# Kernel tuning notes

Hardware: AMD Instinct MI355X
Metric: run time of the kernel (lower is better)

Reference implementation:

```python
import jax, jax.numpy as jnp
import numpy as np

EMBED_DIM = 1024
NUM_HEADS = 16
HEAD_DIM = EMBED_DIM // NUM_HEADS


def setup_inputs() -> dict:
    key = jax.random.key(0)
    ks = jax.random.split(key, 10)
    B, S, E = 2, 2048, EMBED_DIM
    scale = 1.0 / np.sqrt(E)
    x = jax.random.normal(ks[0], (B, S, E), dtype=jnp.float32)
    mask = jax.random.randint(ks[1], (B, 1, S, S), 0, 2, dtype=jnp.int32)
    # Linear weights stored as [in, out] (transposed torch layout for x @ W)
    Wq = jax.random.normal(ks[2], (E, E), dtype=jnp.float32) * scale
    bq = jnp.zeros((E,), dtype=jnp.float32)
    Wk = jax.random.normal(ks[3], (E, E), dtype=jnp.float32) * scale
    bk = jnp.zeros((E,), dtype=jnp.float32)
    Wv = jax.random.normal(ks[4], (E, E), dtype=jnp.float32) * scale
    bv = jnp.zeros((E,), dtype=jnp.float32)
    Wo = jax.random.normal(ks[5], (E, E), dtype=jnp.float32) * scale
    bo = jnp.zeros((E,), dtype=jnp.float32)
    return {"x": x, "mask": mask, "Wq": Wq, "bq": bq, "Wk": Wk, "bk": bk,
            "Wv": Wv, "bv": bv, "Wo": Wo, "bo": bo}


def _heads(t, B, S):
    # [B, S, E] -> [B, H, S, Dh]
    return t.reshape(B, S, NUM_HEADS, HEAD_DIM).transpose(0, 2, 1, 3)


def reference(x, mask, Wq, bq, Wk, bk, Wv, bv, Wo, bo):
    B, S, E = x.shape
    q = _heads(x @ Wq + bq, B, S)
    k = _heads(x @ Wk + bk, B, S)
    v = _heads(x @ Wv + bv, B, S)
    inv_sqrt_dk = 1.0 / jnp.sqrt(jnp.asarray(HEAD_DIM, dtype=x.dtype))
    # scores: [B, H, S, S]
    scores = jnp.einsum('bhqd,bhkd->bhqk', q, k) * inv_sqrt_dk
    scores = jnp.where(mask == 0, jnp.asarray(-1e9, dtype=scores.dtype), scores)
    p = jax.nn.softmax(scores, axis=-1)
    ctx = jnp.einsum('bhqk,bhkd->bhqd', p, v)  # [B, H, S, Dh]
    ctx = ctx.transpose(0, 2, 1, 3).reshape(B, S, E)
    return ctx @ Wo + bo
```

## Files before the change

### kernel.cpp

```cpp
#include <hip/hip_runtime.h>

typedef float f32x4 __attribute__((ext_vector_type(4)));
typedef short s16x8 __attribute__((ext_vector_type(8)));
typedef unsigned short u16;
typedef unsigned short u16x4 __attribute__((ext_vector_type(4)));
typedef unsigned int u32x2 __attribute__((ext_vector_type(2)));

#define DI __device__ __forceinline__

constexpr int B_ = 2, S_ = 2048, E_ = 1024, H_ = 16, DH = 64, M_ = B_ * S_;
constexpr float QSCALE = 0.125f * 1.4426950408889634f;

DI u16 f2bf(float f) {
    unsigned u = __float_as_uint(f);
    u += 0x7fffu + ((u >> 16) & 1u);
    return (u16)(u >> 16);
}

DI unsigned cvtpk(float lo, float hi) {
    unsigned r;
    asm("v_cvt_pk_bf16_f32 %0, %1, %2" : "=v"(r) : "v"(lo), "v"(hi));
    return r;
}

DI float max3f(float a, float b, float c) {
    float r;
    asm("v_max3_f32 %0, %1, %2, %3" : "=v"(r) : "v"(a), "v"(b), "v"(c));
    return r;
}

DI void mfma(f32x4& d, s16x8 a, s16x8 b) {
    asm("v_mfma_f32_16x16x32_bf16 %0, %1, %2, %0" : "+v"(d) : "v"(a), "v"(b));
}

typedef __attribute__((address_space(1))) const void gas_cv;
typedef __attribute__((address_space(3))) void las_v;
DI void gl16(const void* g, void* l) {
    __builtin_amdgcn_global_load_lds((gas_cv*)g, (las_v*)l, 16, 0, 0);
}

__global__ __launch_bounds__(256) void prep(const float* __restrict__ x,
                                            u16* __restrict__ xb,
                                            const float* __restrict__ Wq,
                                            const float* __restrict__ Wk,
                                            const float* __restrict__ Wv,
                                            const float* __restrict__ Wo,
                                            u16* __restrict__ Wqkvt,
                                            u16* __restrict__ Wot,
                                            const int* __restrict__ mask,
                                            u32x2* __restrict__ mc) {
    __shared__ float t[64][65];
    const int bid = blockIdx.x;
    if (bid < 4096) {
        int i = bid * 256 + threadIdx.x;
        float4 v = ((const float4*)x)[i];
        u16x4 o;
        o.x = f2bf(v.x); o.y = f2bf(v.y); o.z = f2bf(v.z); o.w = f2bf(v.w);
        ((u16x4*)xb)[i] = o;
    } else if (bid < 5120) {
        const int wb = bid - 4096, w = wb >> 8, rem = wb & 255;
        const float* in = (w == 0) ? Wq : (w == 1) ? Wk : (w == 2) ? Wv : Wo;
        u16* out = (w == 3) ? Wot : Wqkvt + w * 1024 * 1024;
        const int k0 = (rem & 15) * 64, n0 = (rem >> 4) * 64;
        const int tx = threadIdx.x & 63, ty = threadIdx.x >> 6;
#pragma unroll
        for (int i = 0; i < 16; i++) {
            int r = i * 4 + ty;
            t[r][tx] = in[(k0 + r) * E_ + n0 + tx];
        }
        __syncthreads();
#pragma unroll
        for (int i = 0; i < 16; i++) {
            int r = i * 4 + ty;
            out[(n0 + r) * E_ + k0 + tx] = f2bf(t[tx][r]);
        }
    } else {
        const int bq = bid - 5120;
        const int b = bq >> 7, qt = bq & 127;
        const int tid = threadIdx.x, lane = tid & 63, w = tid >> 6;
        const int lr = lane & 15, g = lane >> 4;
        const int* mrow = mask + ((size_t)(b * S_ + qt * 16 + lr)) * S_;
        u32x2* ob = mc + (size_t)bq * 32 * 4 * 64 + lane;
        for (int kt = w; kt < 32; kt += 4) {
#pragma unroll
            for (int n = 0; n < 4; n++) {
                int4 mv = *(const int4*)(mrow + kt * 64 + n * 16 + g * 4);
                u32x2 e;
                e.x = (mv.x ? 0xFFFFu : 0u) | (mv.y ? 0xFFFF0000u : 0u);
                e.y = (mv.z ? 0xFFFFu : 0u) | (mv.w ? 0xFFFF0000u : 0u);
                ob[(kt * 4 + n) * 64] = e;
            }
        }
    }
}

template <int MODE>
__global__ __launch_bounds__(256) void proj(const u16* __restrict__ A,
                                            const u16* __restrict__ Bt,
                                            const float* __restrict__ b0,
                                            const float* __restrict__ b1,
                                            const float* __restrict__ b2,
                                            u16* __restrict__ Qh, u16* __restrict__ Kh,
                                            u16* __restrict__ Vt,
                                            float* __restrict__ of) {
    __shared__ u16 sA[128 * 64], sB[128 * 64];
    const int tid = threadIdx.x, lane = tid & 63, wid = tid >> 6;
    const int g = lane >> 4, lr = lane & 15;
    const int wr = wid >> 1, wc = wid & 1;
    constexpr int NCT = (MODE == 0) ? 24 : 8;
    const int nblk = (M_ / 128) * NCT;
    const int cpx = nblk / 8;
    const int sw = (blockIdx.x & 7) * cpx + (blockIdx.x >> 3);
    const int rt = sw / NCT, ct = sw % NCT;
    const int row0 = rt * 128, col0 = ct * 128;

    const int srow = lane >> 3;
    const int scol = (lane & 7) * 8;

    f32x4 acc[4][4] = {};
    for (int kt = 0; kt < E_ / 64; kt++) {
        int k0 = kt * 64;
        __syncthreads();
#pragma unroll
        for (int j = 0; j < 4; j++) {
            int r = wid * 32 + j * 8;
            gl16(A  + (size_t)(row0 + r + srow) * E_ + k0 + scol, sA + r * 64);
            gl16(Bt + (size_t)(col0 + r + srow) * E_ + k0 + scol, sB + r * 64);
        }
        __syncthreads();
#pragma unroll
        for (int kk = 0; kk < 2; kk++) {
            s16x8 af[4], bfr[4];
#pragma unroll
            for (int m = 0; m < 4; m++)
                af[m] = *(const s16x8*)(sA + (wr * 64 + m * 16 + lr) * 64 + kk * 32 + g * 8);
#pragma unroll
            for (int n = 0; n < 4; n++)
                bfr[n] = *(const s16x8*)(sB + (wc * 64 + n * 16 + lr) * 64 + kk * 32 + g * 8);
            __builtin_amdgcn_s_setprio(1);
#pragma unroll
            for (int m = 0; m < 4; m++)
#pragma unroll
                for (int n = 0; n < 4; n++) mfma(acc[m][n], af[m], bfr[n]);
            __builtin_amdgcn_s_setprio(0);
        }
    }

    if constexpr (MODE == 3) {
#pragma unroll
        for (int n = 0; n < 4; n++) {
            int c = col0 + wc * 64 + n * 16 + lr;
            float bb = b0[c];
#pragma unroll
            for (int m = 0; m < 4; m++) {
                int rb = row0 + wr * 64 + m * 16 + g * 4;
#pragma unroll
                for (int i = 0; i < 4; i++) of[(size_t)(rb + i) * E_ + c] = acc[m][n][i] + bb;
            }
        }
    } else {
        const int region = col0 >> 10;
        const float* bias = region == 0 ? b0 : (region == 1 ? b1 : b2);
        const float scl = region == 0 ? QSCALE : 1.0f;
        u16* dst = region == 0 ? Qh : Kh;
#pragma unroll
        for (int n = 0; n < 4; n++) {
            int ccol = (col0 & 1023) + wc * 64 + n * 16 + lr;
            float bb = bias[ccol];
            int h = ccol >> 6, dh = ccol & 63;
#pragma unroll
            for (int m = 0; m < 4; m++) {
                int rb = row0 + wr * 64 + m * 16 + g * 4;
                int b = rb >> 11, s = rb & (S_ - 1);
                if (region == 2) {
                    u16x4 pk;
                    pk.x = f2bf(acc[m][n][0] + bb);
                    pk.y = f2bf(acc[m][n][1] + bb);
                    pk.z = f2bf(acc[m][n][2] + bb);
                    pk.w = f2bf(acc[m][n][3] + bb);
                    *(u16x4*)(Vt + ((size_t)((b * H_ + h) * DH + dh)) * S_ + s) = pk;
                } else {
#pragma unroll
                    for (int i = 0; i < 4; i++) {
                        int r = rb + i, bb2 = r >> 11, s2 = r & (S_ - 1);
                        dst[((size_t)((bb2 * H_ + h) * S_) + s2) * DH + dh] =
                            f2bf((acc[m][n][i] + bb) * scl);
                    }
                }
            }
        }
    }
}

__global__ __launch_bounds__(256, 4) void attn(const u16* __restrict__ Q,
                                               const u16* __restrict__ K,
                                               const u16* __restrict__ V,
                                               const u32x2* __restrict__ mc,
                                               u16* __restrict__ ctx) {
    __shared__ u16 sK[2][64 * 64];
    __shared__ u16 sV[2][64 * 64];
    __shared__ u16 sP[4][16 * 64];
    const int tid = threadIdx.x, lane = tid & 63, wid = tid >> 6;
    const int g = lane >> 4, lr = lane & 15, swz = lr & 7;
    const int swg = (blockIdx.x & 7) * 128 + (blockIdx.x >> 3);
    const int q0 = (swg & 31) * 64, h = (swg >> 5) & 15, b = swg >> 9;
    const u16* qb = Q + ((size_t)(b * H_ + h) * S_ + q0) * DH;
    const u16* kb = K + (size_t)(b * H_ + h) * S_ * DH;
    const u16* vb = V + (size_t)(b * H_ + h) * DH * S_;
    const u32x2* mcb = mc + (size_t)(b * 128 + (q0 >> 4) + wid) * 32 * 4 * 64 + lane;
    u16* sPw = sP[wid];

    s16x8 qf[2];
#pragma unroll
    for (int dc = 0; dc < 2; dc++)
        qf[dc] = *(const s16x8*)(qb + (wid * 16 + lr) * DH + dc * 32 + g * 8);

    const u16 ov = (lr == 0) ? (u16)0x3F80 : (u16)0;
    s16x8 ones;
#pragma unroll
    for (int i = 0; i < 8; i++) ones[i] = (short)ov;

    f32x4 o[4] = {};
    f32x4 ol = {};
    float mrun = -3e38f;
    s16x8 kv[2], vv[2];
    u32x2 mmc[4], mmn[4];

#pragma unroll
    for (int p = 0; p < 2; p++) {
        int L = p * 256 + tid;
        kv[p] = *(const s16x8*)(kb + (L >> 3) * DH + (L & 7) * 8);
        vv[p] = *(const s16x8*)(vb + (L >> 3) * S_ + (L & 7) * 8);
    }
#pragma unroll
    for (int n = 0; n < 4; n++) mmc[n] = mcb[n * 64];
#pragma unroll
    for (int p = 0; p < 2; p++) {
        int L = p * 256 + tid;
        int rr = L >> 3, cc = L & 7;
        *(s16x8*)(sK[0] + rr * 64 + (cc ^ (rr & 7)) * 8) = kv[p];
        *(s16x8*)(sV[0] + rr * 64 + (cc ^ (rr & 7)) * 8) = vv[p];
    }
    __syncthreads();

    int cur = 0;
    for (int kt = 0; kt < S_ / 64; kt++) {
        const int k0 = kt * 64;
        if (kt < S_ / 64 - 1) {
            const int kn = k0 + 64;
#pragma unroll
            for (int n = 0; n < 4; n++) mmn[n] = mcb[((kt + 1) * 4 + n) * 64];
#pragma unroll
            for (int p = 0; p < 2; p++) {
                int L = p * 256 + tid;
                kv[p] = *(const s16x8*)(kb + (kn + (L >> 3)) * DH + (L & 7) * 8);
                vv[p] = *(const s16x8*)(vb + (L >> 3) * S_ + kn + (L & 7) * 8);
            }
        }

        const u16* sKc = sK[cur];
        const u16* sVc = sV[cur];
        f32x4 sc[4];
        __builtin_amdgcn_s_setprio(1);
#pragma unroll
        for (int n = 0; n < 4; n++) {
            const u16* kr = sKc + (n * 16 + lr) * 64;
            s16x8 kf0 = *(const s16x8*)(kr + (g ^ swz) * 8);
            s16x8 kf1 = *(const s16x8*)(kr + ((4 + g) ^ swz) * 8);
            f32x4 z = {0.f, 0.f, 0.f, 0.f};
            sc[n] = z;
            mfma(sc[n], kf0, qf[0]);
            mfma(sc[n], kf1, qf[1]);
        }
        __builtin_amdgcn_s_setprio(0);

        float t0 = max3f(sc[0][0], sc[0][1], sc[0][2]);
        float t1 = max3f(sc[0][3], sc[1][0], sc[1][1]);
        float t2 = max3f(sc[1][2], sc[1][3], sc[2][0]);
        float t3 = max3f(sc[2][1], sc[2][2], sc[2][3]);
        float t4 = max3f(sc[3][0], sc[3][1], sc[3][2]);
        float vm = fmaxf(max3f(max3f(t0, t1, sc[3][3]), t3, t4), t2);
        vm = fmaxf(vm, __shfl_xor(vm, 16));
        vm = fmaxf(vm, __shfl_xor(vm, 32));
        if (!__all(vm <= mrun + 8.f)) {
            float fac = __builtin_amdgcn_exp2f(mrun - vm);
            mrun = fmaxf(mrun, vm);
#pragma unroll
            for (int n = 0; n < 4; n++) o[n] *= fac;
            ol *= fac;
        }
#pragma unroll
        for (int n = 0; n < 4; n++) {
            u32x2 wp;
            wp.x = cvtpk(__builtin_amdgcn_exp2f(sc[n][0] - mrun),
                         __builtin_amdgcn_exp2f(sc[n][1] - mrun)) & mmc[n].x;
            wp.y = cvtpk(__builtin_amdgcn_exp2f(sc[n][2] - mrun),
                         __builtin_amdgcn_exp2f(sc[n][3] - mrun)) & mmc[n].y;
            int unit = (n * 2 + (g >> 1)) ^ swz;
            *(u32x2*)(sPw + lr * 64 + unit * 8 + (g & 1) * 4) = wp;
        }
        __builtin_amdgcn_s_setprio(1);
#pragma unroll
        for (int kc = 0; kc < 2; kc++) {
            s16x8 pb = *(const s16x8*)(sPw + lr * 64 + ((kc * 4 + g) ^ swz) * 8);
            mfma(ol, ones, pb);
#pragma unroll
            for (int n = 0; n < 4; n++) {
                int rv = n * 16 + lr;
                s16x8 vf = *(const s16x8*)(sVc + rv * 64 + ((kc * 4 + g) ^ (rv & 7)) * 8);
                mfma(o[n], vf, pb);
            }
        }
        __builtin_amdgcn_s_setprio(0);
        if (kt < S_ / 64 - 1) {
#pragma unroll
            for (int p = 0; p < 2; p++) {
                int L = p * 256 + tid;
                int rr = L >> 3, cc = L & 7;
                *(s16x8*)(sK[cur ^ 1] + rr * 64 + (cc ^ (rr & 7)) * 8) = kv[p];
                *(s16x8*)(sV[cur ^ 1] + rr * 64 + (cc ^ (rr & 7)) * 8) = vv[p];
            }
#pragma unroll
            for (int n = 0; n < 4; n++) mmc[n] = mmn[n];
            __syncthreads();
            cur ^= 1;
        }
    }
    {
        float lsum = __shfl(ol[0], lr);
        float inv = 1.f / lsum;
#pragma unroll
        for (int n = 0; n < 4; n++) {
            u16x4 pk;
#pragma unroll
            for (int i = 0; i < 4; i++) pk[i] = f2bf(o[n][i] * inv);
            *(u16x4*)(sPw + lr * 64 + n * 16 + g * 4) = pk;
        }
#pragma unroll
        for (int half = 0; half < 2; half++) {
            int rr = half * 8 + (lane >> 3);
            s16x8 v = *(const s16x8*)(sPw + rr * 64 + (lane & 7) * 8);
            int q = q0 + wid * 16 + rr;
            *(s16x8*)(ctx + ((size_t)(b * S_ + q)) * E_ + h * DH + (lane & 7) * 8) = v;
        }
    }
}


extern "C" void kernel_launch(void* const* d_in, const int* in_sizes, int n_in,
                              void* d_out, int out_size, void* d_ws, size_t ws_size,
                              hipStream_t stream) {
    const float* x  = (const float*)d_in[0];
    const int* mask = (const int*)d_in[1];
    const float* Wq = (const float*)d_in[2]; const float* bq = (const float*)d_in[3];
    const float* Wk = (const float*)d_in[4]; const float* bk = (const float*)d_in[5];
    const float* Wv = (const float*)d_in[6]; const float* bv = (const float*)d_in[7];
    const float* Wo = (const float*)d_in[8]; const float* bo = (const float*)d_in[9];
    float* out = (float*)d_out;

    char* ws = (char*)d_ws;
    u16* xb     = (u16*)(ws);
    u16* Wqkvt  = (u16*)(ws + (8u  << 20));
    u16* Wot    = (u16*)(ws + (14u << 20));
    u16* Qh     = (u16*)(ws + (16u << 20));
    u16* Kh     = (u16*)(ws + (24u << 20));
    u16* Vt     = (u16*)(ws + (32u << 20));
    u16* ctx    = (u16*)(ws + (40u << 20));
    u32x2* mc   = (u32x2*)(ws + (48u << 20));

    prep<<<5376, 256, 0, stream>>>(x, xb, Wq, Wk, Wv, Wo, Wqkvt, Wot, mask, mc);

    proj<0><<<(M_ / 128) * (3072 / 128), 256, 0, stream>>>(xb, Wqkvt, bq, bk, bv,
                                                           Qh, Kh, Vt, nullptr);

    attn<<<(S_ / 64) * H_ * B_, 256, 0, stream>>>(Qh, Kh, Vt, mc, ctx);

    proj<3><<<(M_ / 128) * (E_ / 128), 256, 0, stream>>>(ctx, Wot, bo, nullptr, nullptr,
                                                         nullptr, nullptr, nullptr, out);
}
```

Before: 154.2 us.

## Double-buffer LDS tiles in projection GEMM to overlap global loads with MFMA

The projection GEMM now keeps two LDS buffers per operand and issues the global-to-LDS loads for the next K tile before computing on the current one. It waits on the vmcnt counter so that only the current tile's loads must complete. This is meant to hide global memory latency behind the matrix multiplies instead of stalling at each K step. In exchange it doubles LDS use to 64KB per block, which can reduce occupancy, and it relies on hand-placed barriers and waitcnt counts being correct.

```diff
diff --git a/kernel.cpp b/kernel.cpp
--- a/kernel.cpp
+++ b/kernel.cpp
@@ -103,7 +103,7 @@
                                             u16* __restrict__ Qh, u16* __restrict__ Kh,
                                             u16* __restrict__ Vt,
                                             float* __restrict__ of) {
-    __shared__ u16 sA[128 * 64], sB[128 * 64];
+    __shared__ u16 sA[2][128 * 64], sB[2][128 * 64];
     const int tid = threadIdx.x, lane = tid & 63, wid = tid >> 6;
     const int g = lane >> 4, lr = lane & 15;
     const int wr = wid >> 1, wc = wid & 1;
@@ -117,32 +117,47 @@
     const int srow = lane >> 3;
     const int scol = (lane & 7) * 8;
 
-    f32x4 acc[4][4] = {};
-    for (int kt = 0; kt < E_ / 64; kt++) {
+    auto STAGE = [&](int kt, int buf) {
         int k0 = kt * 64;
-        __syncthreads();
 #pragma unroll
         for (int j = 0; j < 4; j++) {
             int r = wid * 32 + j * 8;
-            gl16(A  + (size_t)(row0 + r + srow) * E_ + k0 + scol, sA + r * 64);
-            gl16(Bt + (size_t)(col0 + r + srow) * E_ + k0 + scol, sB + r * 64);
-        }
-        __syncthreads();
+            gl16(A  + (size_t)(row0 + r + srow) * E_ + k0 + scol, sA[buf] + r * 64);
+            gl16(Bt + (size_t)(col0 + r + srow) * E_ + k0 + scol, sB[buf] + r * 64);
+        }
+    };
+
+    f32x4 acc[4][4] = {};
+    STAGE(0, 0);
+    for (int kt = 0; kt < 16; kt++) {
+        const int pb = kt & 1;
+        if (kt < 15) {
+            STAGE(kt + 1, pb ^ 1);
+            asm volatile("s_waitcnt vmcnt(8)" ::: "memory");
+        } else {
+            asm volatile("s_waitcnt vmcnt(0)" ::: "memory");
+        }
+        __builtin_amdgcn_s_barrier();
+        __builtin_amdgcn_sched_barrier(0);
 #pragma unroll
         for (int kk = 0; kk < 2; kk++) {
             s16x8 af[4], bfr[4];
 #pragma unroll
             for (int m = 0; m < 4; m++)
-                af[m] = *(const s16x8*)(sA + (wr * 64 + m * 16 + lr) * 64 + kk * 32 + g * 8);
+                af[m] = *(const s16x8*)(sA[pb] + (wr * 64 + m * 16 + lr) * 64 + kk * 32 + g * 8);
 #pragma unroll
             for (int n = 0; n < 4; n++)
-                bfr[n] = *(const s16x8*)(sB + (wc * 64 + n * 16 + lr) * 64 + kk * 32 + g * 8);
+                bfr[n] = *(const s16x8*)(sB[pb] + (wc * 64 + n * 16 + lr) * 64 + kk * 32 + g * 8);
             __builtin_amdgcn_s_setprio(1);
 #pragma unroll
             for (int m = 0; m < 4; m++)
 #pragma unroll
                 for (int n = 0; n < 4; n++) mfma(acc[m][n], af[m], bfr[n]);
             __builtin_amdgcn_s_setprio(0);
+        }
+        if (kt < 15) {
+            __builtin_amdgcn_sched_barrier(0);
+            __builtin_amdgcn_s_barrier();
         }
     }
 
```

Measured after the change: 169.4 us. +9.9%, slower.
